# Optimization experiments

Measured on AMD Instinct MI355X. Metric: run time of the kernel, lower is better.

The kernel has to match this reference:

```python
import jax, jax.numpy as jnp
import numpy as np
import math

B, S, E, H = 2, 2048, 1024, 16
D = E // H  # d_attn = 64
SCALE = 1.0 / math.sqrt(D)


def setup_inputs() -> dict:
    key = jax.random.key(0)
    ks = jax.random.split(key, 5)
    std = 0.02
    return {
        "q": jax.random.normal(ks[0], (B, S, E), dtype=jnp.float32),
        "Wq": jax.random.normal(ks[1], (E, H * D), dtype=jnp.float32) * std,
        "Wk": jax.random.normal(ks[2], (E, H * D), dtype=jnp.float32) * std,
        "Wv": jax.random.normal(ks[3], (E, H * D), dtype=jnp.float32) * std,
        "Wo": jax.random.normal(ks[4], (H * D, E), dtype=jnp.float32) * std,
        "gamma": jnp.ones((H,), dtype=jnp.float32),
    }


def reference(q, Wq, Wk, Wv, Wo, gamma):
    Bq, Sq, _ = q.shape
    # projections -> [B, H, S, D]
    qh = (q @ Wq).reshape(Bq, Sq, H, D).transpose(0, 2, 1, 3)
    kh = (q @ Wk).reshape(Bq, Sq, H, D).transpose(0, 2, 1, 3)
    vh = (q @ Wv).reshape(Bq, Sq, H, D).transpose(0, 2, 1, 3)
    # RBF distance scores: ||q||^2 - 2 q.k + ||k||^2, clamped at 0
    q_norm = jnp.sum(qh * qh, axis=-1, keepdims=True)          # [B,H,S,1]
    k_norm = jnp.sum(kh * kh, axis=-1, keepdims=True)          # [B,H,S,1]
    qk = jnp.einsum("bhsd,bhtd->bhst", qh, kh)                # [B,H,S,S]
    dist = jnp.maximum(q_norm - 2.0 * qk + jnp.swapaxes(k_norm, -2, -1), 0.0)
    scores = jnp.exp(-gamma[None, :, None, None] * SCALE * dist)
    # source: masked_fill(causal_mask == 0, 0) with mask = triu(ones, 1)
    # -> scores kept only on the STRICT upper triangle (faithful to source)
    mask = jnp.triu(jnp.ones((Sq, Sq), dtype=bool), k=1)
    scores = jnp.where(mask, scores, 0.0)
    out = jnp.einsum("bhst,bhtd->bhsd", scores, vh)            # [B,H,S,D]
    out = out.transpose(0, 2, 1, 3).reshape(Bq, Sq, H * D)
    return out @ Wo
```

## Files before the change

### kernel.cpp

```cpp
#include <hip/hip_runtime.h>
#include <stdint.h>

#define SCALE 0.125f
#define GSL_C 0.180336880111f

typedef short s16x8 __attribute__((ext_vector_type(8)));
typedef float f32x4 __attribute__((ext_vector_type(4)));
typedef float f32x16 __attribute__((ext_vector_type(16)));

__device__ __forceinline__ unsigned short f2bf(float x){
  union { float f; unsigned int u; } v; v.f = x;
  unsigned int r = v.u + 0x7fffu + ((v.u >> 16) & 1u);
  return (unsigned short)(r >> 16);
}
__device__ __forceinline__ float bf2f(unsigned short u){
  union { unsigned int u; float f; } v; v.u = ((unsigned int)u) << 16;
  return v.f;
}
__device__ __forceinline__ f32x4 mfma16(s16x8 a, s16x8 b, f32x4 c){
  return __builtin_amdgcn_mfma_f32_16x16x32_bf16(a, b, c, 0, 0, 0);
}
__device__ __forceinline__ f32x16 mfma32(s16x8 a, s16x8 b, f32x16 c){
  return __builtin_amdgcn_mfma_f32_32x32x16_bf16(a, b, c, 0, 0, 0);
}
__device__ __forceinline__ void gld_lds16(const void* g, void* l){
  __builtin_amdgcn_global_load_lds(
      (const __attribute__((address_space(1))) unsigned int*)g,
      (__attribute__((address_space(3))) unsigned int*)l, 16, 0, 0);
}
__device__ __forceinline__ unsigned int cvtpk(float lo, float hi){
  unsigned int r;
  asm("v_cvt_pk_bf16_f32 %0, %1, %2" : "=v"(r) : "v"(lo), "v"(hi));
  return r;
}
__device__ __forceinline__ void plswap(unsigned int &a, unsigned int &b){
  asm("v_permlane32_swap_b32 %0, %1" : "+v"(a), "+v"(b));
}

__global__ __launch_bounds__(256) void cast_kernel(const float* __restrict__ in,
                                                   unsigned short* __restrict__ out){
  int i = blockIdx.x*256 + threadIdx.x;
  const float4* p = (const float4*)in + (size_t)i*2;
  float4 a = p[0], b = p[1];
  unsigned short t[8] = {f2bf(a.x),f2bf(a.y),f2bf(a.z),f2bf(a.w),
                         f2bf(b.x),f2bf(b.y),f2bf(b.z),f2bf(b.w)};
  *(s16x8*)(out + (size_t)i*8) = *(const s16x8*)t;
}

__global__ __launch_bounds__(256) void wtrans_kernel(const float* __restrict__ W0,
    const float* __restrict__ W1, const float* __restrict__ W2, const float* __restrict__ W3,
    unsigned short* __restrict__ Wt){
  const float* src = (blockIdx.z==0)?W0:(blockIdx.z==1)?W1:(blockIdx.z==2)?W2:W3;
  unsigned short* dst = Wt + (size_t)blockIdx.z*1048576;
  int k0 = blockIdx.x*64, n0 = blockIdx.y*64;
  __shared__ unsigned short tile[64*72];
  int tid = threadIdx.x;
  int r = tid>>2, c = (tid&3)*16;
  const float* p = src + (size_t)(k0+r)*1024 + n0 + c;
  #pragma unroll
  for (int j=0;j<16;j++) tile[r*72 + c + j] = f2bf(p[j]);
  __syncthreads();
  int n = tid>>2, kc = (tid&3)*16;
  unsigned short o[16];
  #pragma unroll
  for (int j=0;j<16;j++) o[j] = tile[(kc+j)*72 + n];
  *(s16x8*)&dst[(size_t)(n0+n)*1024 + k0 + kc]     = *(const s16x8*)o;
  *(s16x8*)&dst[(size_t)(n0+n)*1024 + k0 + kc + 8] = *(const s16x8*)(o+8);
}

__global__ __launch_bounds__(256) void vtrans_kernel(const unsigned short* __restrict__ Vh,
    unsigned short* __restrict__ VtG){
  int bh = blockIdx.y, t0 = blockIdx.x*64;
  __shared__ unsigned short tile[64*72];
  int tid = threadIdx.x;
  #pragma unroll
  for (int p=0;p<2;p++){
    int idx = p*2048 + tid*8;
    int r = idx>>6, c = idx&63;
    *(s16x8*)&tile[r*72 + c] = *(const s16x8*)&Vh[((size_t)bh*2048 + t0 + r)*64 + c];
  }
  __syncthreads();
  #pragma unroll
  for (int p=0;p<2;p++){
    int idx = p*2048 + tid*8;
    int d = idx>>6, c = idx&63;
    unsigned short o[8];
    #pragma unroll
    for (int j=0;j<8;j++) o[j] = tile[(c+j)*72 + d];
    *(s16x8*)&VtG[((size_t)bh*64 + d)*2048 + t0 + c] = *(const s16x8*)o;
  }
}

template<int MODE>
__global__ __launch_bounds__(512) void gemm_db(const unsigned short* __restrict__ A,
    const unsigned short* __restrict__ Bt, unsigned short* __restrict__ outH,
    float* __restrict__ outF, float* __restrict__ qn, float* __restrict__ kn,
    const float* __restrict__ gamma){
  __shared__ short As[16384];
  __shared__ short Bs[16384];
  int tid = threadIdx.x;
  int w = tid>>6, l = tid&63;
  int lm = l & 15, hi = l >> 4;
  int wr = w>>1, wc = w&1;
  int m0 = blockIdx.x*128, n0 = blockIdx.y*128;

  const unsigned short* Bz;
  int bn0;
  if constexpr (MODE==1){ Bz = Bt + (size_t)(n0>>10)*1048576; bn0 = n0 & 1023; }
  else                  { Bz = Bt; bn0 = n0; }

  f32x4 acc[2][4];
  #pragma unroll
  for (int r=0;r<2;r++)
    #pragma unroll
    for (int c=0;c<4;c++){ f32x4 z = {0.f,0.f,0.f,0.f}; acc[r][c] = z; }

  int rsub = l>>3, csw = ((l&7) ^ (l>>3))*8;
  const unsigned short* gA = A  + (size_t)(m0  + w*16 + rsub)*1024 + csw;
  const unsigned short* gB = Bz + (size_t)(bn0 + w*16 + rsub)*1024 + csw;
  short* lA = As + w*1024;
  short* lB = Bs + w*1024;

  int ch0 = ((hi)     ^ (lm&7))*8;
  int ch1 = ((4 + hi) ^ (lm&7))*8;

  gld_lds16(gA,        lA);
  gld_lds16(gA + 8192, lA + 512);
  gld_lds16(gB,        lB);
  gld_lds16(gB + 8192, lB + 512);
  __syncthreads();

  const int NKT = 16;
  int buf = 0;
  for (int kt=0; kt<NKT; ++kt){
    if (kt+1 < NKT){
      const unsigned short* a = gA + (size_t)(kt+1)*64;
      const unsigned short* b = gB + (size_t)(kt+1)*64;
      short* dA = As + (buf^1)*8192 + w*1024;
      short* dB = Bs + (buf^1)*8192 + w*1024;
      gld_lds16(a,        dA);
      gld_lds16(a + 8192, dA + 512);
      gld_lds16(b,        dB);
      gld_lds16(b + 8192, dB + 512);
    }
    const short* curA = As + buf*8192;
    const short* curB = Bs + buf*8192;
    s16x8 af[2][2], bfv[4][2];
    #pragma unroll
    for (int r=0;r<2;r++){
      int ro = (wr*32 + r*16 + lm)*64;
      af[r][0] = *(const s16x8*)(curA + ro + ch0);
      af[r][1] = *(const s16x8*)(curA + ro + ch1);
    }
    #pragma unroll
    for (int c=0;c<4;c++){
      int ro = (wc*64 + c*16 + lm)*64;
      bfv[c][0] = *(const s16x8*)(curB + ro + ch0);
      bfv[c][1] = *(const s16x8*)(curB + ro + ch1);
    }
    __builtin_amdgcn_s_setprio(1);
    #pragma unroll
    for (int s=0;s<2;s++)
      #pragma unroll
      for (int r=0;r<2;r++)
        #pragma unroll
        for (int c=0;c<4;c++)
          acc[r][c] = mfma16(af[r][s], bfv[c][s], acc[r][c]);
    __builtin_amdgcn_s_setprio(0);
    __syncthreads();
    buf ^= 1;
  }

  if constexpr (MODE==0){
    #pragma unroll
    for (int r=0;r<2;r++)
      #pragma unroll
      for (int c=0;c<4;c++)
        #pragma unroll
        for (int i=0;i<4;i++){
          int m = m0 + wr*32 + r*16 + hi*4 + i;
          int n = n0 + wc*64 + c*16 + lm;
          outF[(size_t)m*1024 + n] = acc[r][c][i];
        }
  } else {
    int z = n0 >> 10;
    unsigned short* oz = outH + (size_t)z*4194304;
    #pragma unroll
    for (int r=0;r<2;r++){
      #pragma unroll
      for (int i=0;i<4;i++){
        int m = m0 + wr*32 + r*16 + hi*4 + i;
        int bq = m >> 11, sq = m & 2047;
        float nrm = 0.f;
        #pragma unroll
        for (int c=0;c<4;c++){
          int nn = (n0 & 1023) + wc*64 + c*16 + lm;
          int hq = nn >> 6, dq = nn & 63;
          int bh = bq*16 + hq;
          unsigned short bv = f2bf(acc[r][c][i]);
          oz[((size_t)bh*2048 + sq)*64 + dq] = bv;
          float vf = bf2f(bv);
          nrm = fmaf(vf, vf, nrm);
        }
        if (z < 2){
          nrm += __shfl_xor(nrm, 1);
          nrm += __shfl_xor(nrm, 2);
          nrm += __shfl_xor(nrm, 4);
          nrm += __shfl_xor(nrm, 8);
          if (lm == 0){
            int hq = ((n0 & 1023) + wc*64) >> 6;
            float gsl_h = gamma[hq] * GSL_C;
            float* dst = z ? kn : qn;
            dst[(size_t)(bq*16 + hq)*2048 + sq] = nrm * gsl_h;
          }
        }
      }
    }
  }
}

__global__ __launch_bounds__(128, 2) void attn_kernel(const unsigned short* __restrict__ Qh,
    const unsigned short* __restrict__ Kh, const unsigned short* __restrict__ VtG,
    const float* __restrict__ qn, const float* __restrict__ kn,
    const float* __restrict__ gamma, unsigned short* __restrict__ attnO){
  __shared__ short Ks[2][4096];
  __shared__ short Vs[2][4096];

  int bid = blockIdx.x;
  int bh = bid & 31; int b = bh>>4, h = bh&15;
  int rr = bid >> 5;
  int g = rr >> 3, r8 = rr & 7;
  int si = (g==0) ? r8 : (g==1) ? (31-r8) : (g==2) ? (8+r8) : (23-r8);
  int s0 = si*64;
  int tid = threadIdx.x, w = tid>>6, l = tid&63;
  int l31 = l & 31, hi5 = l >> 5, l7 = l & 7;
  float gs2l = 2.f * gamma[h] * GSL_C;

  int q0 = s0 + w*32;
  int qrow = q0 + l31;
  const unsigned short* qb = Qh + ((size_t)bh*2048 + qrow)*64;
  s16x8 qf[4];
  #pragma unroll
  for (int c=0;c<4;c++) qf[c] = *(const s16x8*)(qb + c*16 + hi5*8);
  float gq = -qn[(size_t)bh*2048 + qrow];
  const float* knp = kn + (size_t)bh*2048;

  int chs = (l7 ^ (l>>3))*8;
  const unsigned short* kp0 = Kh  + ((size_t)bh*2048 + s0 + w*32 + (l>>3))*64 + chs;
  const unsigned short* vp0 = VtG + ((size_t)bh*64 + w*32 + (l>>3))*2048 + s0 + chs;

  f32x16 accO0, accO1;
  #pragma unroll
  for (int r=0;r<16;r++){ accO0[r] = 0.f; accO1[r] = 0.f; }

#define STAGE(bufi, dt) { \
    const unsigned short* kp = kp0 + (size_t)(dt)*64; \
    const unsigned short* vp = vp0 + (dt); \
    short* dK = &Ks[bufi][w*2048]; \
    short* dV = &Vs[bufi][w*2048]; \
    gld_lds16(kp,         dK); \
    gld_lds16(kp +  512,  dK + 512); \
    gld_lds16(kp + 1024,  dK + 1024); \
    gld_lds16(kp + 1536,  dK + 1536); \
    gld_lds16(vp,         dV); \
    gld_lds16(vp + 16384, dV + 512); \
    gld_lds16(vp + 32768, dV + 1024); \
    gld_lds16(vp + 49152, dV + 1536); \
  }

  STAGE(0, 0);
  __syncthreads();

  int cur = 0;
  for (int t0 = s0; t0 < 2048; t0 += 64, cur ^= 1){
    if (t0 + 64 < 2048) STAGE(cur^1, t0 + 64 - s0);
    const short* kb = &Ks[cur][0];
    const short* vb = &Vs[cur][0];

    #pragma unroll
    for (int tb=0; tb<2; tb++){
      int tbase = t0 + tb*32 - s0;
      if (tbase + 31 <= w*32) continue;
      f32x16 sc;
      #pragma unroll
      for (int r=0;r<16;r++) sc[r] = 0.f;
      __builtin_amdgcn_s_setprio(1);
      #pragma unroll
      for (int c=0;c<4;c++){
        s16x8 kf = *(const s16x8*)(kb + (tb*32 + l31)*64 + (((2*c + hi5) ^ l7)*8));
        sc = mfma32(kf, qf[c], sc);
      }
      __builtin_amdgcn_s_setprio(0);
      float e[16];
      #pragma unroll
      for (int gg=0; gg<4; gg++){
        float4 knv = *(const float4*)(knp + t0 + tb*32 + gg*8 + hi5*4);
        float ks4[4] = {knv.x, knv.y, knv.z, knv.w};
        #pragma unroll
        for (int i=0;i<4;i++){
          int r = gg*4 + i;
          e[r] = __builtin_amdgcn_exp2f(fminf(fmaf(gs2l, sc[r], gq - ks4[i]), 0.f));
        }
      }
      if (tbase < w*32 + 32){
        #pragma unroll
        for (int r=0;r<16;r++){
          int t = t0 + tb*32 + (r&3) + 8*(r>>2) + 4*hi5;
          e[r] = (t > qrow) ? e[r] : 0.f;
        }
      }
      unsigned int u0 = cvtpk(e[0],  e[1]),  u1 = cvtpk(e[2],  e[3]);
      unsigned int u2 = cvtpk(e[4],  e[5]),  u3 = cvtpk(e[6],  e[7]);
      unsigned int u4 = cvtpk(e[8],  e[9]),  u5 = cvtpk(e[10], e[11]);
      unsigned int u6 = cvtpk(e[12], e[13]), u7 = cvtpk(e[14], e[15]);
      plswap(u0, u2);
      plswap(u1, u3);
      plswap(u4, u6);
      plswap(u5, u7);
      unsigned int f0[4] = {u0, u1, u2, u3};
      unsigned int f1[4] = {u4, u5, u6, u7};
      s16x8 pa0 = *(const s16x8*)f0;
      s16x8 pa1 = *(const s16x8*)f1;
      __builtin_amdgcn_s_setprio(1);
      {
        int cg0 = 2*tb, cg1 = 2*tb + 1;
        s16x8 v00 = *(const s16x8*)(vb + (l31)*64      + (((2*cg0 + hi5) ^ l7)*8));
        s16x8 v01 = *(const s16x8*)(vb + (l31)*64      + (((2*cg1 + hi5) ^ l7)*8));
        s16x8 v10 = *(const s16x8*)(vb + (32 + l31)*64 + (((2*cg0 + hi5) ^ l7)*8));
        s16x8 v11 = *(const s16x8*)(vb + (32 + l31)*64 + (((2*cg1 + hi5) ^ l7)*8));
        accO0 = mfma32(pa0, v00, accO0);
        accO0 = mfma32(pa1, v01, accO0);
        accO1 = mfma32(pa0, v10, accO1);
        accO1 = mfma32(pa1, v11, accO1);
      }
      __builtin_amdgcn_s_setprio(0);
    }
    __syncthreads();
  }
#undef STAGE

  #pragma unroll
  for (int r=0;r<16;r++){
    int s = q0 + (r&3) + 8*(r>>2) + 4*hi5;
    size_t base = ((size_t)b*2048 + s)*1024 + h*64;
    attnO[base + l31]      = f2bf(accO0[r]);
    attnO[base + 32 + l31] = f2bf(accO1[r]);
  }
}

extern "C" void kernel_launch(void* const* d_in, const int* in_sizes, int n_in,
                              void* d_out, int out_size, void* d_ws, size_t ws_size,
                              hipStream_t stream){
  const float* q  = (const float*)d_in[0];
  const float* Wq = (const float*)d_in[1];
  const float* Wk = (const float*)d_in[2];
  const float* Wv = (const float*)d_in[3];
  const float* Wo = (const float*)d_in[4];
  const float* gm = (const float*)d_in[5];
  float* out = (float*)d_out;

  unsigned short* qbf = (unsigned short*)d_ws;
  unsigned short* Wt  = qbf + 4194304;
  unsigned short* Qh  = Wt  + 4194304;
  unsigned short* Kh  = Qh  + 4194304;
  unsigned short* Vh  = Kh  + 4194304;
  unsigned short* Vt  = Vh  + 4194304;
  unsigned short* aO  = Vt  + 4194304;
  float* qn = (float*)(aO + 4194304);
  float* kn = qn + 65536;

  cast_kernel  <<<2048, 256, 0, stream>>>(q, qbf);
  wtrans_kernel<<<dim3(16,16,4), 256, 0, stream>>>(Wq, Wk, Wv, Wo, Wt);
  gemm_db<1>   <<<dim3(32,24), 512, 0, stream>>>(qbf, Wt, Qh, nullptr, qn, kn, gm);
  vtrans_kernel<<<dim3(32,32), 256, 0, stream>>>(Vh, Vt);
  attn_kernel  <<<dim3(1024), 128, 0, stream>>>(Qh, Kh, Vt, qn, kn, gm, aO);
  gemm_db<0>   <<<dim3(32,8), 512, 0, stream>>>(aO, Wt + 3*1048576, nullptr, out, nullptr, nullptr, nullptr);
}
```

Before: 117.6 us.

## Split attention key range into balanced jobs with partial buffers and sum kernel

Replaces the per-64-row-tile attention grid with a static job table of 35 jobs per head. Each job covers a 128-row query tile and a sub-range of key tiles, so the causal triangle is spread evenly across 1120 blocks of 256 threads. Partial outputs go to up to three bf16 buffers, which reuse dead workspace. Unused slots are zero-filled and a new sum3 kernel adds the buffers before the output projection. This trades extra global traffic, an extra launch and bf16 partial-sum rounding for better load balance and occupancy.

```diff
diff --git a/kernel.cpp b/kernel.cpp
--- a/kernel.cpp
+++ b/kernel.cpp
@@ -219,19 +219,33 @@
   }
 }
 
-__global__ __launch_bounds__(128, 2) void attn_kernel(const unsigned short* __restrict__ Qh,
+#define JOB(si,ts,te,buf,zm) ((unsigned int)((si)|((ts)<<4)|((te)<<10)|((buf)<<16)|((zm)<<18)))
+__device__ const unsigned int JOBS[35] = {
+  JOB(0,0,11,0,0),  JOB(0,11,22,1,0), JOB(0,22,32,2,0), JOB(1,2,12,0,0),
+  JOB(1,12,22,1,0), JOB(1,22,32,2,0), JOB(2,4,14,0,0),  JOB(2,14,24,1,0),
+  JOB(11,22,32,0,3),JOB(3,6,15,0,0),  JOB(3,15,24,1,0), JOB(2,24,32,2,0),
+  JOB(3,24,32,2,0), JOB(4,8,16,0,0),  JOB(4,16,24,1,0), JOB(4,24,32,2,0),
+  JOB(5,10,18,0,0), JOB(5,18,26,1,0), JOB(8,16,24,0,2), JOB(8,24,32,1,0),
+  JOB(12,24,32,0,3),JOB(6,12,19,0,0), JOB(6,19,26,1,0), JOB(9,18,25,0,2),
+  JOB(9,25,32,1,0), JOB(5,26,32,2,0), JOB(6,26,32,2,0), JOB(7,14,20,0,0),
+  JOB(7,20,26,1,0), JOB(7,26,32,2,0), JOB(10,20,26,0,2),JOB(10,26,32,1,0),
+  JOB(13,26,32,0,3),JOB(14,28,32,0,3),JOB(15,30,32,0,3)
+};
+
+__global__ __launch_bounds__(256, 4) void attn_kernel(const unsigned short* __restrict__ Qh,
     const unsigned short* __restrict__ Kh, const unsigned short* __restrict__ VtG,
     const float* __restrict__ qn, const float* __restrict__ kn,
-    const float* __restrict__ gamma, unsigned short* __restrict__ attnO){
+    const float* __restrict__ gamma, unsigned short* __restrict__ aO0,
+    unsigned short* __restrict__ aO1, unsigned short* __restrict__ aO2){
   __shared__ short Ks[2][4096];
   __shared__ short Vs[2][4096];
 
   int bid = blockIdx.x;
   int bh = bid & 31; int b = bh>>4, h = bh&15;
-  int rr = bid >> 5;
-  int g = rr >> 3, r8 = rr & 7;
-  int si = (g==0) ? r8 : (g==1) ? (31-r8) : (g==2) ? (8+r8) : (23-r8);
-  int s0 = si*64;
+  unsigned int e = JOBS[bid >> 5];
+  int si2 = e & 15, ts = (e>>4)&63, te = (e>>10)&63, bsel = (e>>16)&3, zm = (e>>18)&3;
+  int s0 = si2*128;
+
   int tid = threadIdx.x, w = tid>>6, l = tid&63;
   int l31 = l & 31, hi5 = l >> 5, l7 = l & 7;
   float gs2l = 2.f * gamma[h] * GSL_C;
@@ -246,34 +260,31 @@
   const float* knp = kn + (size_t)bh*2048;
 
   int chs = (l7 ^ (l>>3))*8;
-  const unsigned short* kp0 = Kh  + ((size_t)bh*2048 + s0 + w*32 + (l>>3))*64 + chs;
-  const unsigned short* vp0 = VtG + ((size_t)bh*64 + w*32 + (l>>3))*2048 + s0 + chs;
+  const unsigned short* kp0 = Kh  + ((size_t)bh*2048 + w*8 + (l>>3))*64 + chs;
+  const unsigned short* vp0 = VtG + ((size_t)bh*64 + w*8 + (l>>3))*2048 + chs;
 
   f32x16 accO0, accO1;
   #pragma unroll
   for (int r=0;r<16;r++){ accO0[r] = 0.f; accO1[r] = 0.f; }
 
-#define STAGE(bufi, dt) { \
-    const unsigned short* kp = kp0 + (size_t)(dt)*64; \
-    const unsigned short* vp = vp0 + (dt); \
-    short* dK = &Ks[bufi][w*2048]; \
-    short* dV = &Vs[bufi][w*2048]; \
-    gld_lds16(kp,         dK); \
-    gld_lds16(kp +  512,  dK + 512); \
-    gld_lds16(kp + 1024,  dK + 1024); \
-    gld_lds16(kp + 1536,  dK + 1536); \
-    gld_lds16(vp,         dV); \
-    gld_lds16(vp + 16384, dV + 512); \
-    gld_lds16(vp + 32768, dV + 1024); \
-    gld_lds16(vp + 49152, dV + 1536); \
-  }
-
-  STAGE(0, 0);
+#define STAGE(bufi, tabs) { \
+    const unsigned short* kp = kp0 + (size_t)(tabs)*64; \
+    const unsigned short* vp = vp0 + (tabs); \
+    short* dK = &Ks[bufi][w*512]; \
+    short* dV = &Vs[bufi][w*512]; \
+    gld_lds16(kp,           dK); \
+    gld_lds16(kp + 32*64,   dK + 2048); \
+    gld_lds16(vp,           dV); \
+    gld_lds16(vp + 32*2048, dV + 2048); \
+  }
+
+  STAGE(0, ts*64);
   __syncthreads();
 
   int cur = 0;
-  for (int t0 = s0; t0 < 2048; t0 += 64, cur ^= 1){
-    if (t0 + 64 < 2048) STAGE(cur^1, t0 + 64 - s0);
+  for (int tt = ts; tt < te; ++tt, cur ^= 1){
+    if (tt + 1 < te) STAGE(cur^1, (tt+1)*64);
+    int t0 = tt*64;
     const short* kb = &Ks[cur][0];
     const short* vb = &Vs[cur][0];
 
@@ -291,7 +302,7 @@
         sc = mfma32(kf, qf[c], sc);
       }
       __builtin_amdgcn_s_setprio(0);
-      float e[16];
+      float ev[16];
       #pragma unroll
       for (int gg=0; gg<4; gg++){
         float4 knv = *(const float4*)(knp + t0 + tb*32 + gg*8 + hi5*4);
@@ -299,20 +310,20 @@
         #pragma unroll
         for (int i=0;i<4;i++){
           int r = gg*4 + i;
-          e[r] = __builtin_amdgcn_exp2f(fminf(fmaf(gs2l, sc[r], gq - ks4[i]), 0.f));
+          ev[r] = __builtin_amdgcn_exp2f(fminf(fmaf(gs2l, sc[r], gq - ks4[i]), 0.f));
         }
       }
       if (tbase < w*32 + 32){
         #pragma unroll
         for (int r=0;r<16;r++){
           int t = t0 + tb*32 + (r&3) + 8*(r>>2) + 4*hi5;
-          e[r] = (t > qrow) ? e[r] : 0.f;
+          ev[r] = (t > qrow) ? ev[r] : 0.f;
         }
       }
-      unsigned int u0 = cvtpk(e[0],  e[1]),  u1 = cvtpk(e[2],  e[3]);
-      unsigned int u2 = cvtpk(e[4],  e[5]),  u3 = cvtpk(e[6],  e[7]);
-      unsigned int u4 = cvtpk(e[8],  e[9]),  u5 = cvtpk(e[10], e[11]);
-      unsigned int u6 = cvtpk(e[12], e[13]), u7 = cvtpk(e[14], e[15]);
+      unsigned int u0 = cvtpk(ev[0],  ev[1]),  u1 = cvtpk(ev[2],  ev[3]);
+      unsigned int u2 = cvtpk(ev[4],  ev[5]),  u3 = cvtpk(ev[6],  ev[7]);
+      unsigned int u4 = cvtpk(ev[8],  ev[9]),  u5 = cvtpk(ev[10], ev[11]);
+      unsigned int u6 = cvtpk(ev[12], ev[13]), u7 = cvtpk(ev[14], ev[15]);
       plswap(u0, u2);
       plswap(u1, u3);
       plswap(u4, u6);
@@ -339,13 +350,41 @@
   }
 #undef STAGE
 
+  unsigned short* aoP = (bsel==0) ? aO0 : (bsel==1) ? aO1 : aO2;
   #pragma unroll
   for (int r=0;r<16;r++){
     int s = q0 + (r&3) + 8*(r>>2) + 4*hi5;
     size_t base = ((size_t)b*2048 + s)*1024 + h*64;
-    attnO[base + l31]      = f2bf(accO0[r]);
-    attnO[base + 32 + l31] = f2bf(accO1[r]);
-  }
+    aoP[base + l31]      = f2bf(accO0[r]);
+    aoP[base + 32 + l31] = f2bf(accO1[r]);
+  }
+  if (zm){
+    s16x8 zz8 = {0,0,0,0,0,0,0,0};
+    int zr = tid >> 1, zc = (tid & 1)*32;
+    size_t zbase = ((size_t)b*2048 + s0 + zr)*1024 + h*64 + zc;
+    if (zm & 1){
+      #pragma unroll
+      for (int j=0;j<4;j++) *(s16x8*)&aO1[zbase + j*8] = zz8;
+    }
+    if (zm & 2){
+      #pragma unroll
+      for (int j=0;j<4;j++) *(s16x8*)&aO2[zbase + j*8] = zz8;
+    }
+  }
+}
+
+__global__ __launch_bounds__(256) void sum3_kernel(unsigned short* __restrict__ a,
+    const unsigned short* __restrict__ bsrc, const unsigned short* __restrict__ csrc){
+  size_t i = ((size_t)blockIdx.x*256 + threadIdx.x)*8;
+  s16x8 va = *(const s16x8*)(a + i);
+  s16x8 vb = *(const s16x8*)(bsrc + i);
+  s16x8 vc = *(const s16x8*)(csrc + i);
+  unsigned short o[8];
+  #pragma unroll
+  for (int j=0;j<8;j++)
+    o[j] = f2bf(bf2f((unsigned short)va[j]) + bf2f((unsigned short)vb[j])
+                + bf2f((unsigned short)vc[j]));
+  *(s16x8*)(a + i) = *(const s16x8*)o;
 }
 
 extern "C" void kernel_launch(void* const* d_in, const int* in_sizes, int n_in,
@@ -369,10 +408,14 @@
   float* qn = (float*)(aO + 4194304);
   float* kn = qn + 65536;
 
+  unsigned short* aO1 = qbf;
+  unsigned short* aO2 = Vh;
+
   cast_kernel  <<<2048, 256, 0, stream>>>(q, qbf);
   wtrans_kernel<<<dim3(16,16,4), 256, 0, stream>>>(Wq, Wk, Wv, Wo, Wt);
   gemm_db<1>   <<<dim3(32,24), 512, 0, stream>>>(qbf, Wt, Qh, nullptr, qn, kn, gm);
   vtrans_kernel<<<dim3(32,32), 256, 0, stream>>>(Vh, Vt);
-  attn_kernel  <<<dim3(1024), 128, 0, stream>>>(Qh, Kh, Vt, qn, kn, gm, aO);
+  attn_kernel  <<<dim3(1120), 256, 0, stream>>>(Qh, Kh, Vt, qn, kn, gm, aO, aO1, aO2);
+  sum3_kernel  <<<dim3(2048), 256, 0, stream>>>(aO, aO1, aO2);
   gemm_db<0>   <<<dim3(32,8), 512, 0, stream>>>(aO, Wt + 3*1048576, nullptr, out, nullptr, nullptr, nullptr);
 }
```

Result: faster. 113.7 us (-3.3%).
